# Kernel optimization log

Hardware: AMD Instinct MI355X
Metric: run time of the kernel (lower is better)

Reference implementation:

```python
import jax, jax.numpy as jnp
import numpy as np

B, L, D = 16384, 32, 128
DIAG_LEN, PROC_LEN, MED_LEN = 100000, 50000, 1000


def setup_inputs() -> dict:
    key = jax.random.key(0)
    ks = jax.random.split(key, 12)
    inp = {
        "diag_codes": jax.random.randint(ks[0], (B, L), 0, DIAG_LEN),
        "proc_codes": jax.random.randint(ks[1], (B, L), 0, PROC_LEN),
        "prev_diag_codes": jax.random.randint(ks[2], (B, L), 0, DIAG_LEN),
        "prev_proc_codes": jax.random.randint(ks[3], (B, L), 0, PROC_LEN),
        # learned parameters (torch Linear convention: W[out,in], y = x @ W.T + b)
        "diag_emb": jax.random.normal(ks[4], (DIAG_LEN, D), jnp.float32) * 0.02,
        "proc_emb": jax.random.normal(ks[5], (PROC_LEN, D), jnp.float32) * 0.02,
        "W1": jax.random.normal(ks[6], (D, 2 * D), jnp.float32) * 0.02,
        "b1": jnp.zeros((D,), jnp.float32),
        "W2": jax.random.normal(ks[7], (256, 2 * D), jnp.float32) * 0.02,
        "b2": jnp.zeros((256,), jnp.float32),
        "W3": jax.random.normal(ks[8], (MED_LEN, 256), jnp.float32) * 0.02,
        "b3": jnp.zeros((MED_LEN,), jnp.float32),
    }
    return inp


def _bag_sum(table, idx):
    # EmbeddingBag('sum'): gather [B,L,D] then reduce over codes -> [B,D]
    return jnp.take(table, idx, axis=0).sum(axis=1)


def reference(diag_codes, proc_codes, prev_diag_codes, prev_proc_codes,
              diag_emb, proc_emb, W1, b1, W2, b2, W3, b3):
    emb_d = _bag_sum(diag_emb, diag_codes)            # [B,128]
    emb_p = _bag_sum(proc_emb, proc_codes)            # [B,128]
    prev_d = _bag_sum(diag_emb, prev_diag_codes)      # [B,128]
    prev_p = _bag_sum(proc_emb, prev_proc_codes)      # [B,128]

    # health_net = Linear(256->128) + Dropout (identity in eval mode)
    cur = jnp.concatenate([emb_d, emb_p], axis=1) @ W1.T + b1     # [B,128]
    prev = jnp.concatenate([prev_d, prev_p], axis=1) @ W1.T + b1  # [B,128]

    rep = jnp.concatenate([cur, prev], axis=1)        # [B,256]
    h = jax.nn.relu(rep @ W2.T + b2)                  # [B,256]
    return jax.nn.sigmoid(h @ W3.T + b3)              # [B,med_len]
```

## Files before the change

### kernel.cpp

```cpp
#include <hip/hip_runtime.h>
#include <hip/hip_bf16.h>
#include <math.h>

#define NB 16384
#define MED 1000
#define MD 100000
#define MP 50000
#define TDBLK 782
#define TPBLK 391
#define NTR (TDBLK + TPBLK)
#define NCV 1280
#define FP8_SCALE 4096.0f
#define FP8_INV   (1.0f / 4096.0f)

typedef __bf16 bf16x8 __attribute__((ext_vector_type(8)));
typedef float  f32x4  __attribute__((ext_vector_type(4)));
typedef float  f32x2  __attribute__((ext_vector_type(2)));
typedef unsigned short u16;
typedef unsigned int   u32;
typedef unsigned char  u8;

__device__ __forceinline__ u16 f2bf(float f) {
    union { float f; u32 u; } v; v.f = f;
    u32 r = v.u + 0x7fffu + ((v.u >> 16) & 1u);
    return (u16)(r >> 16);
}

__global__ __launch_bounds__(256) void prep_kernel(
    const float* __restrict__ Ed, const float* __restrict__ Ep,
    const float* __restrict__ W1,
    const float* __restrict__ W2, const float* __restrict__ W3,
    u8* __restrict__ Td, u8* __restrict__ Tp,
    u16* __restrict__ W2b, u16* __restrict__ W3b)
{
    __shared__ u16 w1s[128 * 132];
    const int bid = blockIdx.x, tid = threadIdx.x;

    if (bid >= NTR) {
        int i = (bid - NTR) * 256 + tid;
        if (i < 65536) { W2b[i] = f2bf(W2[i]); return; }
        i -= 65536;
        if (i < 262144) W3b[i] = (i < MED * 256) ? f2bf(W3[i]) : (u16)0;
        return;
    }

    int blk = bid;
    const float* E; u8* T; int M, koff;
    if (blk < TDBLK) { E = Ed; T = Td; M = MD; koff = 0; }
    else             { blk -= TDBLK; E = Ep; T = Tp; M = MP; koff = 128; }

    for (int idx = tid; idx < 4096; idx += 256) {
        const int row = idx >> 5, c4 = idx & 31;
        const float4 v = *(const float4*)(W1 + row * 256 + koff + c4 * 4);
        u16* d = &w1s[row * 132 + c4 * 4];
        d[0] = f2bf(v.x); d[1] = f2bf(v.y); d[2] = f2bf(v.z); d[3] = f2bf(v.w);
    }
    __syncthreads();

    const int wave = tid >> 6, lane = tid & 63;
    const int quad = lane >> 4, l16 = lane & 15;
    const int n0 = blk * 128 + wave * 32;
    const float* bP0 = E + (size_t)min(n0 + l16,      M - 1) * 128 + quad * 8;
    const float* bP1 = E + (size_t)min(n0 + 16 + l16, M - 1) * 128 + quad * 8;

    f32x4 acc[8][2];
    #pragma unroll
    for (int mt = 0; mt < 8; ++mt) {
        acc[mt][0] = (f32x4){0.f,0.f,0.f,0.f};
        acc[mt][1] = (f32x4){0.f,0.f,0.f,0.f};
    }

    #pragma unroll
    for (int ks = 0; ks < 4; ++ks) {
        union { bf16x8 v; u16 s[8]; } b0, b1;
        const float4 f0 = *(const float4*)(bP0 + ks * 32);
        const float4 f1 = *(const float4*)(bP0 + ks * 32 + 4);
        const float4 g0 = *(const float4*)(bP1 + ks * 32);
        const float4 g1 = *(const float4*)(bP1 + ks * 32 + 4);
        b0.s[0]=f2bf(f0.x); b0.s[1]=f2bf(f0.y); b0.s[2]=f2bf(f0.z); b0.s[3]=f2bf(f0.w);
        b0.s[4]=f2bf(f1.x); b0.s[5]=f2bf(f1.y); b0.s[6]=f2bf(f1.z); b0.s[7]=f2bf(f1.w);
        b1.s[0]=f2bf(g0.x); b1.s[1]=f2bf(g0.y); b1.s[2]=f2bf(g0.z); b1.s[3]=f2bf(g0.w);
        b1.s[4]=f2bf(g1.x); b1.s[5]=f2bf(g1.y); b1.s[6]=f2bf(g1.z); b1.s[7]=f2bf(g1.w);
        #pragma unroll
        for (int mt = 0; mt < 8; ++mt) {
            const bf16x8 a = *(const bf16x8*)&w1s[(mt * 16 + l16) * 132 + ks * 32 + quad * 8];
            acc[mt][0] = __builtin_amdgcn_mfma_f32_16x16x32_bf16(a, b0.v, acc[mt][0], 0, 0, 0);
            acc[mt][1] = __builtin_amdgcn_mfma_f32_16x16x32_bf16(a, b1.v, acc[mt][1], 0, 0, 0);
        }
    }

    #pragma unroll
    for (int nt = 0; nt < 2; ++nt) {
        const int rn = n0 + nt * 16 + l16;
        if (rn < M) {
            u8* rowp = T + (size_t)rn * 128 + quad * 4;
            #pragma unroll
            for (int mt = 0; mt < 8; ++mt) {
                const f32x4 a = acc[mt][nt];
                int p = __builtin_amdgcn_cvt_pk_fp8_f32(a[0] * FP8_SCALE, a[1] * FP8_SCALE, 0, 0);
                p = __builtin_amdgcn_cvt_pk_fp8_f32(a[2] * FP8_SCALE, a[3] * FP8_SCALE, p, 1);
                *(u32*)(rowp + mt * 16) = (u32)p;
            }
        }
    }
}

__global__ __launch_bounds__(256) void gather_rep(
    const int* __restrict__ diag, const int* __restrict__ proc,
    const int* __restrict__ pdiag, const int* __restrict__ pproc,
    const u8* __restrict__ Td, const u8* __restrict__ Tp,
    const float* __restrict__ b1, u16* __restrict__ rep)
{
    __shared__ int   sidx[8 * 4 * 33];
    __shared__ float sred[8][2][8][16];
    const int t = threadIdx.x;

    for (int i = t; i < 1024; i += 256) {
        const int s = i >> 7, bg = (i >> 5) & 3, l = i & 31;
        const int* cp = (bg == 0) ? diag : (bg == 1) ? proc : (bg == 2) ? pdiag : pproc;
        sidx[(s * 4 + bg) * 33 + l] = cp[(blockIdx.x * 8 + s) * 32 + l];
    }
    __syncthreads();

    const int sub = t >> 5, bag = (t >> 3) & 3, lc = t & 7;
    const u8* tbl = (bag & 1) ? Tp : Td;
    const int* myidx = &sidx[(sub * 4 + bag) * 33];

    f32x2 s[8];
    #pragma unroll
    for (int i = 0; i < 8; ++i) s[i] = (f32x2){0.f, 0.f};

    uint4 va[8], vb[8];
    #pragma unroll
    for (int j = 0; j < 8; ++j)
        va[j] = *(const uint4*)(tbl + (size_t)myidx[j] * 128 + lc * 16);
    #pragma unroll
    for (int j = 0; j < 8; ++j)
        vb[j] = *(const uint4*)(tbl + (size_t)myidx[8 + j] * 128 + lc * 16);

#define CONSUME(V) do { \
    _Pragma("unroll") \
    for (int j = 0; j < 8; ++j) { \
        s[0] += __builtin_amdgcn_cvt_pk_f32_fp8((int)V[j].x, 0); \
        s[1] += __builtin_amdgcn_cvt_pk_f32_fp8((int)V[j].x, 1); \
        s[2] += __builtin_amdgcn_cvt_pk_f32_fp8((int)V[j].y, 0); \
        s[3] += __builtin_amdgcn_cvt_pk_f32_fp8((int)V[j].y, 1); \
        s[4] += __builtin_amdgcn_cvt_pk_f32_fp8((int)V[j].z, 0); \
        s[5] += __builtin_amdgcn_cvt_pk_f32_fp8((int)V[j].z, 1); \
        s[6] += __builtin_amdgcn_cvt_pk_f32_fp8((int)V[j].w, 0); \
        s[7] += __builtin_amdgcn_cvt_pk_f32_fp8((int)V[j].w, 1); \
    } } while (0)

    {
        uint4 tmp[8];
        #pragma unroll
        for (int j = 0; j < 8; ++j)
            tmp[j] = *(const uint4*)(tbl + (size_t)myidx[16 + j] * 128 + lc * 16);
        CONSUME(va);
        #pragma unroll
        for (int j = 0; j < 8; ++j) va[j] = tmp[j];
    }
    {
        uint4 tmp[8];
        #pragma unroll
        for (int j = 0; j < 8; ++j)
            tmp[j] = *(const uint4*)(tbl + (size_t)myidx[24 + j] * 128 + lc * 16);
        CONSUME(vb);
        #pragma unroll
        for (int j = 0; j < 8; ++j) vb[j] = tmp[j];
    }
    CONSUME(va);
    CONSUME(vb);
#undef CONSUME

    const int half = bag >> 1;
    if (bag & 1) {
        float* dst = &sred[sub][half][lc][0];
        #pragma unroll
        for (int i = 0; i < 4; ++i)
            *(f32x4*)(dst + i * 4) = (f32x4){s[2*i].x, s[2*i].y, s[2*i+1].x, s[2*i+1].y};
    }
    __syncthreads();
    if (!(bag & 1)) {
        const float* par = &sred[sub][half][lc][0];
        const float* bp  = b1 + lc * 16;
        u32 o[8];
        #pragma unroll
        for (int i = 0; i < 8; ++i) {
            const float e0 = (s[i].x + par[2*i])   * FP8_INV + bp[2*i];
            const float e1 = (s[i].y + par[2*i+1]) * FP8_INV + bp[2*i+1];
            o[i] = (u32)f2bf(e0) | ((u32)f2bf(e1) << 16);
        }
        const int b = blockIdx.x * 8 + sub;
        u16* dst = rep + (size_t)b * 256 + half * 128 + lc * 16;
        *(uint4*)dst       = make_uint4(o[0], o[1], o[2], o[3]);
        *(uint4*)(dst + 8) = make_uint4(o[4], o[5], o[6], o[7]);
    }
}

__global__ __launch_bounds__(256) void gemm2(
    const u16* __restrict__ rep, const u16* __restrict__ W2b,
    const float* __restrict__ b2, u16* __restrict__ h)
{
    const int wave = threadIdx.x >> 6, lane = threadIdx.x & 63;
    const int quad = lane >> 4, l16 = lane & 15;
    const int mBase = blockIdx.x * 32;
    const int nBase = wave * 64;
    const u16* aP0 = rep + (size_t)(mBase + l16) * 256 + quad * 8;
    const u16* aP1 = aP0 + 16 * 256;
    const u16* wP  = W2b + (size_t)(nBase + l16) * 256 + quad * 8;

    f32x4 acc[2][4];
    #pragma unroll
    for (int mt = 0; mt < 2; ++mt)
        #pragma unroll
        for (int nt = 0; nt < 4; ++nt) acc[mt][nt] = (f32x4){0.f,0.f,0.f,0.f};

    bf16x8 a0 = *(const bf16x8*)(aP0);
    bf16x8 a1 = *(const bf16x8*)(aP1);
    bf16x8 b[4];
    #pragma unroll
    for (int nt = 0; nt < 4; ++nt) b[nt] = *(const bf16x8*)(wP + nt * 4096);

    #pragma unroll
    for (int ks = 0; ks < 8; ++ks) {
        bf16x8 a0n = a0, a1n = a1, bn[4];
        #pragma unroll
        for (int nt = 0; nt < 4; ++nt) bn[nt] = b[nt];
        if (ks < 7) {
            a0n = *(const bf16x8*)(aP0 + (ks + 1) * 32);
            a1n = *(const bf16x8*)(aP1 + (ks + 1) * 32);
            #pragma unroll
            for (int nt = 0; nt < 4; ++nt)
                bn[nt] = *(const bf16x8*)(wP + nt * 4096 + (ks + 1) * 32);
        }
        #pragma unroll
        for (int nt = 0; nt < 4; ++nt) {
            acc[0][nt] = __builtin_amdgcn_mfma_f32_16x16x32_bf16(a0, b[nt], acc[0][nt], 0, 0, 0);
            acc[1][nt] = __builtin_amdgcn_mfma_f32_16x16x32_bf16(a1, b[nt], acc[1][nt], 0, 0, 0);
        }
        a0 = a0n; a1 = a1n;
        #pragma unroll
        for (int nt = 0; nt < 4; ++nt) b[nt] = bn[nt];
    }

    #pragma unroll
    for (int mt = 0; mt < 2; ++mt) {
        const int rowB = mBase + mt * 16 + quad * 4;
        #pragma unroll
        for (int nt = 0; nt < 4; ++nt) {
            const int col = nBase + nt * 16 + l16;
            const float bv = b2[col];
            #pragma unroll
            for (int r = 0; r < 4; ++r) {
                float v = acc[mt][nt][r] + bv;
                v = v > 0.f ? v : 0.f;
                h[(size_t)(rowB + r) * 256 + col] = f2bf(v);
            }
        }
    }
}

__global__ __launch_bounds__(256) void gemm3(
    const u16* __restrict__ h, const u16* __restrict__ W3b,
    const float* __restrict__ b3, float* __restrict__ out)
{
    const int wave = threadIdx.x >> 6, lane = threadIdx.x & 63;
    const int quad = lane >> 4, l16 = lane & 15;
    const int mBase = blockIdx.x * 64 + (wave & 1) * 32;
    const int nBase = blockIdx.y * 128 + (wave >> 1) * 64;
    const u16* aP0 = h + (size_t)(mBase + l16) * 256 + quad * 8;
    const u16* aP1 = aP0 + 16 * 256;
    const u16* wP  = W3b + (size_t)(nBase + l16) * 256 + quad * 8;

    f32x4 acc[2][4];
    #pragma unroll
    for (int mt = 0; mt < 2; ++mt)
        #pragma unroll
        for (int nt = 0; nt < 4; ++nt) acc[mt][nt] = (f32x4){0.f,0.f,0.f,0.f};

    bf16x8 a0 = *(const bf16x8*)(aP0);
    bf16x8 a1 = *(const bf16x8*)(aP1);
    bf16x8 b[4];
    #pragma unroll
    for (int nt = 0; nt < 4; ++nt) b[nt] = *(const bf16x8*)(wP + nt * 4096);

    #pragma unroll
    for (int ks = 0; ks < 8; ++ks) {
        bf16x8 a0n = a0, a1n = a1, bn[4];
        #pragma unroll
        for (int nt = 0; nt < 4; ++nt) bn[nt] = b[nt];
        if (ks < 7) {
            a0n = *(const bf16x8*)(aP0 + (ks + 1) * 32);
            a1n = *(const bf16x8*)(aP1 + (ks + 1) * 32);
            #pragma unroll
            for (int nt = 0; nt < 4; ++nt)
                bn[nt] = *(const bf16x8*)(wP + nt * 4096 + (ks + 1) * 32);
        }
        #pragma unroll
        for (int nt = 0; nt < 4; ++nt) {
            acc[0][nt] = __builtin_amdgcn_mfma_f32_16x16x32_bf16(a0, b[nt], acc[0][nt], 0, 0, 0);
            acc[1][nt] = __builtin_amdgcn_mfma_f32_16x16x32_bf16(a1, b[nt], acc[1][nt], 0, 0, 0);
        }
        a0 = a0n; a1 = a1n;
        #pragma unroll
        for (int nt = 0; nt < 4; ++nt) b[nt] = bn[nt];
    }

    #pragma unroll
    for (int nt = 0; nt < 4; ++nt) {
        const int col = nBase + nt * 16 + l16;
        if (col < MED) {
            const float bv = b3[col];
            #pragma unroll
            for (int mt = 0; mt < 2; ++mt) {
                const int rowB = mBase + mt * 16 + quad * 4;
                #pragma unroll
                for (int r = 0; r < 4; ++r) {
                    const float v = acc[mt][nt][r] + bv;
                    const float e = __expf(-v);
                    out[(size_t)(rowB + r) * MED + col] = __builtin_amdgcn_rcpf(1.0f + e);
                }
            }
        }
    }
}

extern "C" void kernel_launch(void* const* d_in, const int* in_sizes, int n_in,
                              void* d_out, int out_size, void* d_ws, size_t ws_size,
                              hipStream_t stream)
{
    const int*   diag  = (const int*)d_in[0];
    const int*   proc  = (const int*)d_in[1];
    const int*   pdiag = (const int*)d_in[2];
    const int*   pproc = (const int*)d_in[3];
    const float* demb  = (const float*)d_in[4];
    const float* pemb  = (const float*)d_in[5];
    const float* W1    = (const float*)d_in[6];
    const float* b1    = (const float*)d_in[7];
    const float* W2    = (const float*)d_in[8];
    const float* b2    = (const float*)d_in[9];
    const float* W3    = (const float*)d_in[10];
    const float* b3    = (const float*)d_in[11];

    char* ws = (char*)d_ws;
    u8*  Td  = (u8*)ws;
    u8*  Tp  = (u8*)(ws + 12800000);
    u16* rep = (u16*)(ws + 19200000);
    u16* W2b = (u16*)(ws + 27588608);
    u16* W3b = (u16*)(ws + 27719680);
    u16* h   = (u16*)ws;

    prep_kernel<<<NTR + NCV, 256, 0, stream>>>(demb, pemb, W1, W2, W3, Td, Tp, W2b, W3b);
    gather_rep<<<NB / 8, 256, 0, stream>>>(diag, proc, pdiag, pproc, Td, Tp, b1, rep);
    gemm2<<<512, 256, 0, stream>>>(rep, W2b, b2, h);
    gemm3<<<dim3(256, 8), 256, 0, stream>>>(h, W3b, b3, (float*)d_out);
}
```

Measured before the change: 258.4 us.

## Keep weight tiles register-resident in gemm2/gemm3 and stream A rows through them

```diff
diff --git a/kernel.cpp b/kernel.cpp
--- a/kernel.cpp
+++ b/kernel.cpp
@@ -198,130 +198,128 @@
     }
 }
 
-__global__ __launch_bounds__(256) void gemm2(
+__global__ __launch_bounds__(256, 2) void gemm2(
     const u16* __restrict__ rep, const u16* __restrict__ W2b,
     const float* __restrict__ b2, u16* __restrict__ h)
 {
     const int wave = threadIdx.x >> 6, lane = threadIdx.x & 63;
     const int quad = lane >> 4, l16 = lane & 15;
-    const int mBase = blockIdx.x * 32;
-    const int nBase = wave * 64;
-    const u16* aP0 = rep + (size_t)(mBase + l16) * 256 + quad * 8;
-    const u16* aP1 = aP0 + 16 * 256;
-    const u16* wP  = W2b + (size_t)(nBase + l16) * 256 + quad * 8;
-
-    f32x4 acc[2][4];
-    #pragma unroll
-    for (int mt = 0; mt < 2; ++mt)
-        #pragma unroll
-        for (int nt = 0; nt < 4; ++nt) acc[mt][nt] = (f32x4){0.f,0.f,0.f,0.f};
-
-    bf16x8 a0 = *(const bf16x8*)(aP0);
-    bf16x8 a1 = *(const bf16x8*)(aP1);
-    bf16x8 b[4];
-    #pragma unroll
-    for (int nt = 0; nt < 4; ++nt) b[nt] = *(const bf16x8*)(wP + nt * 4096);
-
-    #pragma unroll
-    for (int ks = 0; ks < 8; ++ks) {
-        bf16x8 a0n = a0, a1n = a1, bn[4];
-        #pragma unroll
-        for (int nt = 0; nt < 4; ++nt) bn[nt] = b[nt];
-        if (ks < 7) {
-            a0n = *(const bf16x8*)(aP0 + (ks + 1) * 32);
-            a1n = *(const bf16x8*)(aP1 + (ks + 1) * 32);
+    const int nBase = blockIdx.x * 64;
+    const int mChunk = blockIdx.y * 128;
+
+    bf16x8 w[4][8];
+    #pragma unroll
+    for (int nt = 0; nt < 4; ++nt) {
+        const u16* wP = W2b + (size_t)(nBase + nt * 16 + l16) * 256 + quad * 8;
+        #pragma unroll
+        for (int ks = 0; ks < 8; ++ks) w[nt][ks] = *(const bf16x8*)(wP + ks * 32);
+    }
+    float bv[4];
+    #pragma unroll
+    for (int nt = 0; nt < 4; ++nt) bv[nt] = b2[nBase + nt * 16 + l16];
+
+    const u16* aP = rep + (size_t)(mChunk + wave * 16 + l16) * 256 + quad * 8;
+    bf16x8 a[8];
+    #pragma unroll
+    for (int ks = 0; ks < 8; ++ks) a[ks] = *(const bf16x8*)(aP + ks * 32);
+
+    #pragma unroll 1
+    for (int iter = 0; iter < 2; ++iter) {
+        bf16x8 an[8];
+        if (iter < 1) {
+            const u16* aN = aP + 64 * 256;
+            #pragma unroll
+            for (int ks = 0; ks < 8; ++ks) an[ks] = *(const bf16x8*)(aN + ks * 32);
+        }
+        f32x4 acc[4];
+        #pragma unroll
+        for (int nt = 0; nt < 4; ++nt) acc[nt] = (f32x4){0.f,0.f,0.f,0.f};
+        #pragma unroll
+        for (int ks = 0; ks < 8; ++ks)
             #pragma unroll
             for (int nt = 0; nt < 4; ++nt)
-                bn[nt] = *(const bf16x8*)(wP + nt * 4096 + (ks + 1) * 32);
-        }
-        #pragma unroll
-        for (int nt = 0; nt < 4; ++nt) {
-            acc[0][nt] = __builtin_amdgcn_mfma_f32_16x16x32_bf16(a0, b[nt], acc[0][nt], 0, 0, 0);
-            acc[1][nt] = __builtin_amdgcn_mfma_f32_16x16x32_bf16(a1, b[nt], acc[1][nt], 0, 0, 0);
-        }
-        a0 = a0n; a1 = a1n;
-        #pragma unroll
-        for (int nt = 0; nt < 4; ++nt) b[nt] = bn[nt];
-    }
-
-    #pragma unroll
-    for (int mt = 0; mt < 2; ++mt) {
-        const int rowB = mBase + mt * 16 + quad * 4;
+                acc[nt] = __builtin_amdgcn_mfma_f32_16x16x32_bf16(a[ks], w[nt][ks], acc[nt], 0, 0, 0);
+
+        const int rowB = mChunk + iter * 64 + wave * 16 + quad * 4;
         #pragma unroll
         for (int nt = 0; nt < 4; ++nt) {
             const int col = nBase + nt * 16 + l16;
-            const float bv = b2[col];
             #pragma unroll
             for (int r = 0; r < 4; ++r) {
-                float v = acc[mt][nt][r] + bv;
+                float v = acc[nt][r] + bv[nt];
                 v = v > 0.f ? v : 0.f;
                 h[(size_t)(rowB + r) * 256 + col] = f2bf(v);
             }
         }
-    }
-}
-
-__global__ __launch_bounds__(256) void gemm3(
+        if (iter < 1) {
+            aP += 64 * 256;
+            #pragma unroll
+            for (int ks = 0; ks < 8; ++ks) a[ks] = an[ks];
+        }
+    }
+}
+
+__global__ __launch_bounds__(256, 2) void gemm3(
     const u16* __restrict__ h, const u16* __restrict__ W3b,
     const float* __restrict__ b3, float* __restrict__ out)
 {
     const int wave = threadIdx.x >> 6, lane = threadIdx.x & 63;
     const int quad = lane >> 4, l16 = lane & 15;
-    const int mBase = blockIdx.x * 64 + (wave & 1) * 32;
-    const int nBase = blockIdx.y * 128 + (wave >> 1) * 64;
-    const u16* aP0 = h + (size_t)(mBase + l16) * 256 + quad * 8;
-    const u16* aP1 = aP0 + 16 * 256;
-    const u16* wP  = W3b + (size_t)(nBase + l16) * 256 + quad * 8;
-
-    f32x4 acc[2][4];
-    #pragma unroll
-    for (int mt = 0; mt < 2; ++mt)
-        #pragma unroll
-        for (int nt = 0; nt < 4; ++nt) acc[mt][nt] = (f32x4){0.f,0.f,0.f,0.f};
-
-    bf16x8 a0 = *(const bf16x8*)(aP0);
-    bf16x8 a1 = *(const bf16x8*)(aP1);
-    bf16x8 b[4];
-    #pragma unroll
-    for (int nt = 0; nt < 4; ++nt) b[nt] = *(const bf16x8*)(wP + nt * 4096);
-
-    #pragma unroll
-    for (int ks = 0; ks < 8; ++ks) {
-        bf16x8 a0n = a0, a1n = a1, bn[4];
-        #pragma unroll
-        for (int nt = 0; nt < 4; ++nt) bn[nt] = b[nt];
-        if (ks < 7) {
-            a0n = *(const bf16x8*)(aP0 + (ks + 1) * 32);
-            a1n = *(const bf16x8*)(aP1 + (ks + 1) * 32);
+    const int nBase = blockIdx.x * 64;
+    const int mChunk = blockIdx.y * 512;
+
+    bf16x8 w[4][8];
+    #pragma unroll
+    for (int nt = 0; nt < 4; ++nt) {
+        const u16* wP = W3b + (size_t)(nBase + nt * 16 + l16) * 256 + quad * 8;
+        #pragma unroll
+        for (int ks = 0; ks < 8; ++ks) w[nt][ks] = *(const bf16x8*)(wP + ks * 32);
+    }
+    float bv[4]; int colv[4];
+    #pragma unroll
+    for (int nt = 0; nt < 4; ++nt) {
+        colv[nt] = nBase + nt * 16 + l16;
+        bv[nt] = (colv[nt] < MED) ? b3[colv[nt]] : 0.f;
+    }
+
+    const u16* aP = h + (size_t)(mChunk + wave * 16 + l16) * 256 + quad * 8;
+    bf16x8 a[8];
+    #pragma unroll
+    for (int ks = 0; ks < 8; ++ks) a[ks] = *(const bf16x8*)(aP + ks * 32);
+
+    #pragma unroll 1
+    for (int iter = 0; iter < 8; ++iter) {
+        bf16x8 an[8];
+        if (iter < 7) {
+            const u16* aN = aP + 64 * 256;
+            #pragma unroll
+            for (int ks = 0; ks < 8; ++ks) an[ks] = *(const bf16x8*)(aN + ks * 32);
+        }
+        f32x4 acc[4];
+        #pragma unroll
+        for (int nt = 0; nt < 4; ++nt) acc[nt] = (f32x4){0.f,0.f,0.f,0.f};
+        #pragma unroll
+        for (int ks = 0; ks < 8; ++ks)
             #pragma unroll
             for (int nt = 0; nt < 4; ++nt)
-                bn[nt] = *(const bf16x8*)(wP + nt * 4096 + (ks + 1) * 32);
-        }
+                acc[nt] = __builtin_amdgcn_mfma_f32_16x16x32_bf16(a[ks], w[nt][ks], acc[nt], 0, 0, 0);
+
+        const int rowB = mChunk + iter * 64 + wave * 16 + quad * 4;
         #pragma unroll
         for (int nt = 0; nt < 4; ++nt) {
-            acc[0][nt] = __builtin_amdgcn_mfma_f32_16x16x32_bf16(a0, b[nt], acc[0][nt], 0, 0, 0);
-            acc[1][nt] = __builtin_amdgcn_mfma_f32_16x16x32_bf16(a1, b[nt], acc[1][nt], 0, 0, 0);
-        }
-        a0 = a0n; a1 = a1n;
-        #pragma unroll
-        for (int nt = 0; nt < 4; ++nt) b[nt] = bn[nt];
-    }
-
-    #pragma unroll
-    for (int nt = 0; nt < 4; ++nt) {
-        const int col = nBase + nt * 16 + l16;
-        if (col < MED) {
-            const float bv = b3[col];
-            #pragma unroll
-            for (int mt = 0; mt < 2; ++mt) {
-                const int rowB = mBase + mt * 16 + quad * 4;
+            if (colv[nt] < MED) {
                 #pragma unroll
                 for (int r = 0; r < 4; ++r) {
-                    const float v = acc[mt][nt][r] + bv;
+                    const float v = acc[nt][r] + bv[nt];
                     const float e = __expf(-v);
-                    out[(size_t)(rowB + r) * MED + col] = __builtin_amdgcn_rcpf(1.0f + e);
+                    out[(size_t)(rowB + r) * MED + colv[nt]] = __builtin_amdgcn_rcpf(1.0f + e);
                 }
             }
+        }
+        if (iter < 7) {
+            aP += 64 * 256;
+            #pragma unroll
+            for (int ks = 0; ks < 8; ++ks) a[ks] = an[ks];
         }
     }
 }
@@ -353,6 +351,6 @@
 
     prep_kernel<<<NTR + NCV, 256, 0, stream>>>(demb, pemb, W1, W2, W3, Td, Tp, W2b, W3b);
     gather_rep<<<NB / 8, 256, 0, stream>>>(diag, proc, pdiag, pproc, Td, Tp, b1, rep);
-    gemm2<<<512, 256, 0, stream>>>(rep, W2b, b2, h);
-    gemm3<<<dim3(256, 8), 256, 0, stream>>>(h, W3b, b3, (float*)d_out);
-}
+    gemm2<<<dim3(4, 128), 256, 0, stream>>>(rep, W2b, b2, h);
+    gemm3<<<dim3(16, 32), 256, 0, stream>>>(h, W3b, b3, (float*)d_out);
+}
```

After: 241.5 us. -6.5%, faster.
